# Optimization experiments

Measured on AMD Instinct MI355X. Metric: run time of the kernel, lower is better.

Reference implementation:

```python
import jax, jax.numpy as jnp
import numpy as np

D_MODEL = 1024
N_HEADS = 16
D_K = D_MODEL // N_HEADS
ROPE_BASE = 10000.0


def _rope_cos_sin(seq_len, dim):
    # matches calc_rope_theta: freqs over even indices of head dim
    freqs = jnp.arange(0, dim, 2, dtype=jnp.float32) / dim
    inv_freq = 1.0 / (ROPE_BASE ** freqs)                      # [dim/2]
    pos = jnp.arange(seq_len, dtype=jnp.float32)               # [S]
    ang = pos[:, None] * inv_freq[None, :]                     # [S, dim/2]
    return jnp.cos(ang), jnp.sin(ang)


def _apply_rope(x, cos, sin):
    # x: [N, S, dk]; complex pairs are consecutive elements (view_as_complex)
    x0 = x[..., 0::2]
    x1 = x[..., 1::2]
    r = x0 * cos - x1 * sin
    i = x0 * sin + x1 * cos
    return jnp.stack([r, i], axis=-1).reshape(x.shape)


def setup_inputs() -> dict:
    key = jax.random.key(0)
    ks = jax.random.split(key, 11)
    B, S, D = 4, 1024, D_MODEL
    w = lambda k: jax.random.normal(k, (D, D), dtype=jnp.float32) * 0.02
    b = lambda k: jax.random.normal(k, (D,), dtype=jnp.float32) * 0.02
    return {
        "q": jax.random.normal(ks[0], (B, S, D), dtype=jnp.float32),
        "k": jax.random.normal(ks[1], (B, S, D), dtype=jnp.float32),
        "v": jax.random.normal(ks[2], (B, S, D), dtype=jnp.float32),
        "Wq": w(ks[3]), "bq": b(ks[4]),
        "Wk": w(ks[5]), "bk": b(ks[6]),
        "Wv": w(ks[7]), "bv": b(ks[8]),
        "Wo": w(ks[9]), "bo": b(ks[10]),
    }


def reference(q, k, v, Wq, bq, Wk, bk, Wv, bv, Wo, bo):
    B, S, D = q.shape
    H, dk = N_HEADS, D_K
    qp = (q @ Wq + bq).reshape(B, S, H, dk)
    kp = (k @ Wk + bk).reshape(B, S, H, dk)
    vp = (v @ Wv + bv).reshape(B, S, H, dk)

    cos, sin = _rope_cos_sin(S, dk)
    # Faithful to source: raw reshape (B,S,H,dk)->(-1,S,dk) before RoPE
    qp = _apply_rope(qp.reshape(-1, S, dk), cos, sin).reshape(B, S, H, dk)
    kp = _apply_rope(kp.reshape(-1, S, dk), cos, sin).reshape(B, S, H, dk)

    qh = qp.transpose(0, 2, 1, 3)  # [B,H,S,dk]
    kh = kp.transpose(0, 2, 1, 3)
    vh = vp.transpose(0, 2, 1, 3)

    scores = jnp.einsum("bhqd,bhkd->bhqk", qh, kh) / jnp.sqrt(jnp.float32(dk))
    attn = jax.nn.softmax(scores, axis=-1)
    out = jnp.einsum("bhqk,bhkd->bhqd", attn, vh)
    out = out.transpose(0, 2, 1, 3).reshape(B, S, D)
    return out @ Wo + bo
```

## Files before the change

### kernel.cpp

```cpp
#include <hip/hip_runtime.h>

typedef __attribute__((ext_vector_type(8))) short bf16x8;
typedef __attribute__((ext_vector_type(4))) short short4v;
typedef __attribute__((ext_vector_type(4))) float f32x4;
typedef __attribute__((ext_vector_type(2))) unsigned u32x2;

#define MFMA16x16x32(a, b, c) __builtin_amdgcn_mfma_f32_16x16x32_bf16((a), (b), (c), 0, 0, 0)

__device__ __forceinline__ short f2bf(float f) {
    unsigned u = __builtin_bit_cast(unsigned, f);
    u += 0x7FFFu + ((u >> 16) & 1u);
    return (short)(u >> 16);
}

__device__ __forceinline__ unsigned cvtpk(float lo, float hi) {
    unsigned r;
    asm("v_cvt_pk_bf16_f32 %0, %1, %2" : "=v"(r) : "v"(lo), "v"(hi));
    return r;
}

__device__ __forceinline__ void gl_lds16(const void* g, void* l) {
    __builtin_amdgcn_global_load_lds((__attribute__((address_space(1))) void*)g,
                                     (__attribute__((address_space(3))) void*)l,
                                     16, 0, 0);
}

__device__ __forceinline__ void cvt16(const float* __restrict__ p, bf16x8& lo, bf16x8& hi) {
    f32x4 a = *(const f32x4*)(p);
    f32x4 b = *(const f32x4*)(p + 4);
    f32x4 c = *(const f32x4*)(p + 8);
    f32x4 d = *(const f32x4*)(p + 12);
#pragma unroll
    for (int i = 0; i < 4; ++i) {
        lo[i]     = f2bf(a[i]);
        lo[i + 4] = f2bf(b[i]);
        hi[i]     = f2bf(c[i]);
        hi[i + 4] = f2bf(d[i]);
    }
}

__global__ __launch_bounds__(256) void cvt3(const float* __restrict__ x0,
                                            const float* __restrict__ x1,
                                            const float* __restrict__ x2,
                                            short* __restrict__ y) {
    int sel = blockIdx.y;
    const float* x = sel == 0 ? x0 : (sel == 1 ? x1 : x2);
    short* yy = y + (size_t)sel * (1 << 22);
    int i = (blockIdx.x * 256 + threadIdx.x) * 16;
    bf16x8 lo, hi;
    cvt16(x + i, lo, hi);
    *(bf16x8*)(yy + i)     = lo;
    *(bf16x8*)(yy + i + 8) = hi;
}

__global__ __launch_bounds__(256) void transW4(const float* __restrict__ w0,
                                               const float* __restrict__ w1,
                                               const float* __restrict__ w2,
                                               const float* __restrict__ w3,
                                               short* __restrict__ wt) {
    __shared__ short t[64][80];
    int z = blockIdx.z;
    const float* W = z == 0 ? w0 : (z == 1 ? w1 : (z == 2 ? w2 : w3));
    short* Wt = wt + (size_t)z * (1 << 20);
    int bx = blockIdx.x, by = blockIdx.y;
    int tid = threadIdx.x;
    int sr = tid >> 2, sc = (tid & 3) * 16;
    bf16x8 lo, hi;
    cvt16(W + (by * 64 + sr) * 1024 + bx * 64 + sc, lo, hi);
    *(bf16x8*)&t[sr][sc]     = lo;
    *(bf16x8*)&t[sr][sc + 8] = hi;
    __syncthreads();
    bf16x8 o0, o1;
#pragma unroll
    for (int i = 0; i < 8; ++i) {
        o0[i] = t[sc + i][sr];
        o1[i] = t[sc + 8 + i][sr];
    }
    short* dst = Wt + (bx * 64 + sr) * 1024 + by * 64 + sc;
    *(bf16x8*)(dst)     = o0;
    *(bf16x8*)(dst + 8) = o1;
}

template <int MODE, int NZ>
__global__ __launch_bounds__(256) void gemm128(const short* __restrict__ A0,
                                               const short* __restrict__ A1,
                                               const short* __restrict__ Bt0,
                                               const short* __restrict__ Bt1,
                                               const float* __restrict__ b0,
                                               const float* __restrict__ b1,
                                               void* __restrict__ d0,
                                               void* __restrict__ d1) {
    __shared__ short As[2][128 * 64];
    __shared__ short Bs[2][128 * 64];
    const int K = 1024;
    int flat = blockIdx.x;
    int xcd = flat & 7, j = flat >> 3;
    int bm = xcd * 4 + (j & 3);
    int bn = (j >> 2) & 7;
    int z  = (NZ == 2) ? (j >> 5) : 0;
    const short* A    = z ? A1 : A0;
    const short* Bt   = z ? Bt1 : Bt0;
    const float* bias = z ? b1 : b0;
    void* dstv        = z ? d1 : d0;

    int tid = threadIdx.x;
    int wave = tid >> 6, lane = tid & 63;
    int quad = lane >> 4, l16 = lane & 15;
    int wm = (wave >> 1) * 64, wn = (wave & 1) * 64;

    f32x4 acc[4][4] = {};

    auto stage = [&](int b, int kb) {
#pragma unroll
        for (int jj = 0; jj < 4; ++jj) {
            int c = jj * 256 + tid;
            gl_lds16(A + (bm * 128 + (c >> 3)) * K + kb + (c & 7) * 8, &As[b][c * 8]);
        }
#pragma unroll
        for (int jj = 0; jj < 4; ++jj) {
            int c = jj * 256 + tid;
            gl_lds16(Bt + (bn * 128 + (c >> 3)) * K + kb + (c & 7) * 8, &Bs[b][c * 8]);
        }
    };

    stage(0, 0);
    __syncthreads();

    for (int kb = 0; kb < K; kb += 64) {
        int cur = (kb >> 6) & 1;
        if (kb + 64 < K) stage(cur ^ 1, kb + 64);
#pragma unroll
        for (int ks = 0; ks < 2; ++ks) {
            bf16x8 bf[4];
#pragma unroll
            for (int ni = 0; ni < 4; ++ni)
                bf[ni] = *(const bf16x8*)&Bs[cur][(wn + ni * 16 + l16) * 64 + ks * 32 + quad * 8];
#pragma unroll
            for (int mi = 0; mi < 4; ++mi) {
                bf16x8 af = *(const bf16x8*)&As[cur][(wm + mi * 16 + l16) * 64 + ks * 32 + quad * 8];
#pragma unroll
                for (int ni = 0; ni < 4; ++ni)
                    acc[mi][ni] = MFMA16x16x32(af, bf[ni], acc[mi][ni]);
            }
        }
        __syncthreads();
    }

    int row0 = bm * 128 + wm;
    int col0 = bn * 128 + wn;
#pragma unroll
    for (int mi = 0; mi < 4; ++mi) {
#pragma unroll
        for (int ni = 0; ni < 4; ++ni) {
            int gn = col0 + ni * 16 + l16;
            float bv = bias[gn];
            f32x4 c = acc[mi][ni];
            if constexpr (MODE == 0) {
                short* dst = (short*)dstv;
                int h = gn >> 6, dd = gn & 63;
                float inv = exp2f(-(float)(dd >> 1) * 0.41524101186092029f);
#pragma unroll
                for (int r = 0; r < 4; ++r) {
                    int gm = row0 + mi * 16 + quad * 4 + r;
                    int s = gm & 1023, b = gm >> 10;
                    int p = ((s << 4) + h) & 1023;
                    float val = c[r] + bv;
                    float partner = __shfl_xor(val, 1);
                    float sn, cs;
                    __sincosf((float)p * inv, &sn, &cs);
                    float res = (dd & 1) ? fmaf(partner, sn, val * cs)
                                         : fmaf(val, cs, -(partner * sn));
                    dst[((b * 16 + h) * 1024 + s) * 64 + dd] = f2bf(res);
                }
            } else if constexpr (MODE == 2) {
                short* dst = (short*)dstv;
                int h = gn >> 6, dd = gn & 63;
                int gm0 = row0 + mi * 16 + quad * 4;
                int s0 = gm0 & 1023, b = gm0 >> 10;
                short4v pack;
#pragma unroll
                for (int r = 0; r < 4; ++r) pack[r] = f2bf(c[r] + bv);
                *(short4v*)&dst[((b * 16 + h) * 64 + dd) * 1024 + s0] = pack;
            } else {
                float* dst = (float*)dstv;
#pragma unroll
                for (int r = 0; r < 4; ++r) {
                    int gm = row0 + mi * 16 + quad * 4 + r;
                    dst[gm * 1024 + gn] = c[r] + bv;
                }
            }
        }
    }
}

__global__ __launch_bounds__(512) void attn_kernel(const short* __restrict__ Qh,
                                                   const short* __restrict__ Kh,
                                                   const short* __restrict__ Vt,
                                                   short* __restrict__ O) {
    __shared__ short Ks[2][32 * 64];
    __shared__ short Vs[2][64 * 32];
    __shared__ short Pl[8][16 * 40];
    int tid = threadIdx.x;
    int wave = tid >> 6, lane = tid & 63;
    int quad = lane >> 4, l16 = lane & 15;
    int bh = blockIdx.x & 63, qt = blockIdx.x >> 6;
    int qrow = qt * 128 + wave * 16;

    const short* Qp = Qh + (bh * 1024 + qrow) * 64;
    bf16x8 aq[2];
#pragma unroll
    for (int kh = 0; kh < 2; ++kh)
        aq[kh] = *(const bf16x8*)&Qp[l16 * 64 + kh * 32 + quad * 8];

    const short* Kp = Kh + bh * 1024 * 64;
    const short* Vp = Vt + bh * 64 * 1024;

    int ck = tid & 255;
    bool isV = tid >= 256;
    int krow = ck >> 3;
    int vrow = ck >> 2;
    int ksrc = krow * 64 + (((ck & 7) ^ (krow & 7)) * 8);
    int vsrc = vrow * 1024 + ((((ck & 3) ^ (vrow & 3) ^ ((vrow >> 2) & 3)) & 3) * 8);

    int ksw  = l16 & 7;
    int vswr = (l16 & 3) ^ ((l16 >> 2) & 3);

    float lsum = 0.f;
    f32x4 oa[4] = {};

    if (!isV) gl_lds16(Kp + ksrc, &Ks[0][ck * 8]);
    else      gl_lds16(Vp + vsrc, &Vs[0][ck * 8]);
    __syncthreads();

    short* Pw = &Pl[wave][0];

    for (int kb = 0; kb < 1024; kb += 32) {
        int cur = (kb >> 5) & 1, nxt = cur ^ 1;
        int kb2 = (kb + 32) & 1023;
        if (!isV) gl_lds16(Kp + kb2 * 64 + ksrc, &Ks[nxt][ck * 8]);
        else      gl_lds16(Vp + kb2 + vsrc,      &Vs[nxt][ck * 8]);

#pragma unroll
        for (int g = 0; g < 2; ++g) {
            f32x4 s = {};
            __builtin_amdgcn_s_setprio(1);
#pragma unroll
            for (int kh = 0; kh < 2; ++kh) {
                bf16x8 ak = *(const bf16x8*)
                    &Ks[cur][(g * 16 + l16) * 64 + (((kh * 4 + quad) ^ ksw) * 8)];
                s = MFMA16x16x32(ak, aq[kh], s);
            }
            __builtin_amdgcn_s_setprio(0);
            float p[4];
#pragma unroll
            for (int r = 0; r < 4; ++r) {
                p[r] = exp2f(s[r] * 0.18033688011112042f);
                lsum += p[r];
            }
            u32x2 w;
            w[0] = cvtpk(p[0], p[1]);
            w[1] = cvtpk(p[2], p[3]);
            *(u32x2*)&Pw[l16 * 40 + g * 16 + quad * 4] = w;
        }

        bf16x8 bv[4];
#pragma unroll
        for (int t = 0; t < 4; ++t)
            bv[t] = *(const bf16x8*)&Vs[cur][(t * 16 + l16) * 32 + ((quad ^ vswr) * 8)];

        asm volatile("s_waitcnt lgkmcnt(0)" ::: "memory");
        bf16x8 ap = *(const bf16x8*)&Pw[l16 * 40 + quad * 8];

        __builtin_amdgcn_s_setprio(1);
#pragma unroll
        for (int t = 0; t < 4; ++t)
            oa[t] = MFMA16x16x32(ap, bv[t], oa[t]);
        __builtin_amdgcn_s_setprio(0);

        __syncthreads();
    }

    lsum += __shfl_xor(lsum, 16);
    lsum += __shfl_xor(lsum, 32);
    float inv[4];
#pragma unroll
    for (int r = 0; r < 4; ++r)
        inv[r] = 1.0f / __shfl(lsum, (lane & 48) + ((lane >> 4) & 3) * 4 + r);

    int b = bh >> 4, h = bh & 15;
#pragma unroll
    for (int t = 0; t < 4; ++t)
#pragma unroll
        for (int r = 0; r < 4; ++r) {
            int s = qrow + quad * 4 + r;
            O[(b * 1024 + s) * 1024 + h * 64 + t * 16 + l16] = f2bf(oa[t][r] * inv[r]);
        }
}

extern "C" void kernel_launch(void* const* d_in, const int* in_sizes, int n_in,
                              void* d_out, int out_size, void* d_ws, size_t ws_size,
                              hipStream_t stream) {
    const float* q  = (const float*)d_in[0];
    const float* k  = (const float*)d_in[1];
    const float* v  = (const float*)d_in[2];
    const float* Wq = (const float*)d_in[3];
    const float* bq = (const float*)d_in[4];
    const float* Wk = (const float*)d_in[5];
    const float* bk = (const float*)d_in[6];
    const float* Wv = (const float*)d_in[7];
    const float* bv = (const float*)d_in[8];
    const float* Wo = (const float*)d_in[9];
    const float* bo = (const float*)d_in[10];

    short* qb   = (short*)d_ws;
    short* kbuf = qb + (4 << 20);
    short* vb   = kbuf + (4 << 20);
    short* wt   = vb + (4 << 20);
    short* wtq  = wt;
    short* wtk  = wt + (1 << 20);
    short* wtv  = wt + (2 << 20);
    short* wto  = wt + (3 << 20);
    short* vt   = qb;
    short* obuf = kbuf;

    short* qh  = (short*)d_out;
    short* kh  = qh + (4 << 20);
    float* out = (float*)d_out;

    cvt3<<<dim3(1024, 3), 256, 0, stream>>>(q, k, v, qb);
    transW4<<<dim3(16, 16, 4), 256, 0, stream>>>(Wq, Wk, Wv, Wo, wt);

    gemm128<0, 2><<<512, 256, 0, stream>>>(qb, kbuf, wtq, wtk, bq, bk, qh, kh);
    gemm128<2, 1><<<256, 256, 0, stream>>>(vb, vb, wtv, wtv, bv, bv, vt, vt);

    attn_kernel<<<512, 512, 0, stream>>>(qh, kh, vt, obuf);

    gemm128<3, 1><<<256, 256, 0, stream>>>(obuf, obuf, wto, wto, bo, bo, out, out);
}
```

Measured before the change: 223.3 us.

## Restructure GEMM to 8 waves with triple-buffered LDS, XOR swizzle, setprio

The projection GEMM moves from 4 to 8 waves per block, so each wave computes a 64x32 sub-tile. LDS goes from double to triple buffering, with a two-stage-ahead prefetch gated by an explicit vmcnt wait and a single barrier per k-step. Global-to-LDS loads use an XOR swizzle on the 16-byte chunk index to avoid LDS bank conflicts on fragment reads. MFMA bursts are wrapped in s_setprio. The goal is to hide load latency and raise occupancy and MFMA issue, at the cost of more LDS per block (96KB) and a hand-tuned waitcnt that may be fragile.

```diff
diff --git a/kernel.cpp b/kernel.cpp
--- a/kernel.cpp
+++ b/kernel.cpp
@@ -82,7 +82,7 @@
 }
 
 template <int MODE, int NZ>
-__global__ __launch_bounds__(256) void gemm128(const short* __restrict__ A0,
+__global__ __launch_bounds__(512) void gemm128(const short* __restrict__ A0,
                                                const short* __restrict__ A1,
                                                const short* __restrict__ Bt0,
                                                const short* __restrict__ Bt1,
@@ -90,8 +90,8 @@
                                                const float* __restrict__ b1,
                                                void* __restrict__ d0,
                                                void* __restrict__ d1) {
-    __shared__ short As[2][128 * 64];
-    __shared__ short Bs[2][128 * 64];
+    __shared__ short As[3][128 * 64];
+    __shared__ short Bs[3][128 * 64];
     const int K = 1024;
     int flat = blockIdx.x;
     int xcd = flat & 7, j = flat >> 3;
@@ -106,44 +106,60 @@
     int tid = threadIdx.x;
     int wave = tid >> 6, lane = tid & 63;
     int quad = lane >> 4, l16 = lane & 15;
-    int wm = (wave >> 1) * 64, wn = (wave & 1) * 64;
-
-    f32x4 acc[4][4] = {};
-
-    auto stage = [&](int b, int kb) {
-#pragma unroll
-        for (int jj = 0; jj < 4; ++jj) {
-            int c = jj * 256 + tid;
-            gl_lds16(A + (bm * 128 + (c >> 3)) * K + kb + (c & 7) * 8, &As[b][c * 8]);
-        }
-#pragma unroll
-        for (int jj = 0; jj < 4; ++jj) {
-            int c = jj * 256 + tid;
-            gl_lds16(Bt + (bn * 128 + (c >> 3)) * K + kb + (c & 7) * 8, &Bs[b][c * 8]);
+    int wm = (wave >> 2) * 64, wn = (wave & 3) * 32;
+    int swr = l16 & 7;
+
+    f32x4 acc[4][2] = {};
+
+    auto stage = [&](int b, int t) {
+        int kb = t * 64;
+#pragma unroll
+        for (int jj = 0; jj < 2; ++jj) {
+            int c = jj * 512 + tid;
+            int row = c >> 3, sl = c & 7;
+            gl_lds16(A + (bm * 128 + row) * K + kb + ((sl ^ (row & 7)) * 8),
+                     &As[b][c * 8]);
+        }
+#pragma unroll
+        for (int jj = 0; jj < 2; ++jj) {
+            int c = jj * 512 + tid;
+            int row = c >> 3, sl = c & 7;
+            gl_lds16(Bt + (bn * 128 + row) * K + kb + ((sl ^ (row & 7)) * 8),
+                     &Bs[b][c * 8]);
         }
     };
 
     stage(0, 0);
-    __syncthreads();
-
-    for (int kb = 0; kb < K; kb += 64) {
-        int cur = (kb >> 6) & 1;
-        if (kb + 64 < K) stage(cur ^ 1, kb + 64);
+    stage(1, 1);
+
+    int cur = 0;
+    for (int t = 0; t < 16; ++t) {
+        asm volatile("s_waitcnt vmcnt(4)" ::: "memory");
+        __builtin_amdgcn_sched_barrier(0);
+        __builtin_amdgcn_s_barrier();
+        __builtin_amdgcn_sched_barrier(0);
+        int pre = cur >= 1 ? cur - 1 : 2;
+        stage(pre, (t + 2) & 15);
 #pragma unroll
         for (int ks = 0; ks < 2; ++ks) {
-            bf16x8 bf[4];
-#pragma unroll
-            for (int ni = 0; ni < 4; ++ni)
-                bf[ni] = *(const bf16x8*)&Bs[cur][(wn + ni * 16 + l16) * 64 + ks * 32 + quad * 8];
-#pragma unroll
-            for (int mi = 0; mi < 4; ++mi) {
-                bf16x8 af = *(const bf16x8*)&As[cur][(wm + mi * 16 + l16) * 64 + ks * 32 + quad * 8];
-#pragma unroll
-                for (int ni = 0; ni < 4; ++ni)
-                    acc[mi][ni] = MFMA16x16x32(af, bf[ni], acc[mi][ni]);
-            }
-        }
-        __syncthreads();
+            bf16x8 bf[2], af[4];
+#pragma unroll
+            for (int ni = 0; ni < 2; ++ni)
+                bf[ni] = *(const bf16x8*)
+                    &Bs[cur][(wn + ni * 16 + l16) * 64 + (((ks * 4 + quad) ^ swr) * 8)];
+#pragma unroll
+            for (int mi = 0; mi < 4; ++mi)
+                af[mi] = *(const bf16x8*)
+                    &As[cur][(wm + mi * 16 + l16) * 64 + (((ks * 4 + quad) ^ swr) * 8)];
+            __builtin_amdgcn_s_setprio(1);
+#pragma unroll
+            for (int mi = 0; mi < 4; ++mi)
+#pragma unroll
+                for (int ni = 0; ni < 2; ++ni)
+                    acc[mi][ni] = MFMA16x16x32(af[mi], bf[ni], acc[mi][ni]);
+            __builtin_amdgcn_s_setprio(0);
+        }
+        cur = cur < 2 ? cur + 1 : 0;
     }
 
     int row0 = bm * 128 + wm;
@@ -151,7 +167,7 @@
 #pragma unroll
     for (int mi = 0; mi < 4; ++mi) {
 #pragma unroll
-        for (int ni = 0; ni < 4; ++ni) {
+        for (int ni = 0; ni < 2; ++ni) {
             int gn = col0 + ni * 16 + l16;
             float bv = bias[gn];
             f32x4 c = acc[mi][ni];
@@ -330,10 +346,10 @@
     cvt3<<<dim3(1024, 3), 256, 0, stream>>>(q, k, v, qb);
     transW4<<<dim3(16, 16, 4), 256, 0, stream>>>(Wq, Wk, Wv, Wo, wt);
 
-    gemm128<0, 2><<<512, 256, 0, stream>>>(qb, kbuf, wtq, wtk, bq, bk, qh, kh);
-    gemm128<2, 1><<<256, 256, 0, stream>>>(vb, vb, wtv, wtv, bv, bv, vt, vt);
+    gemm128<0, 2><<<512, 512, 0, stream>>>(qb, kbuf, wtq, wtk, bq, bk, qh, kh);
+    gemm128<2, 1><<<256, 512, 0, stream>>>(vb, vb, wtv, wtv, bv, bv, vt, vt);
 
     attn_kernel<<<512, 512, 0, stream>>>(qh, kh, vt, obuf);
 
-    gemm128<3, 1><<<256, 256, 0, stream>>>(obuf, obuf, wto, wto, bo, bo, out, out);
-}
+    gemm128<3, 1><<<256, 512, 0, stream>>>(obuf, obuf, wto, wto, bo, bo, out, out);
+}
```

New measurement: 212.2 us. -5.0%, faster.
